# Performance work log

Hardware: AMD Instinct MI355X
Metric: run time of the kernel (lower is better)

Reference implementation:

```python
import jax, jax.numpy as jnp
import numpy as np

B, T, E, H = 4, 2048, 1024, 16
HS = E // H  # head_size = 64
FFN_HID = 100  # hard-coded in FeedForward
EPS = 1e-5


def layernorm(x, g, b):
    mu = jnp.mean(x, axis=-1, keepdims=True)
    var = jnp.mean(jnp.square(x - mu), axis=-1, keepdims=True)
    return (x - mu) * jax.lax.rsqrt(var + EPS) * g + b


def setup_inputs() -> dict:
    key = jax.random.key(0)
    ks = jax.random.split(key, 10)
    s = E ** -0.5
    return {
        "x": jax.random.normal(ks[0], (B, T, E), jnp.float32),
        "wq": jax.random.normal(ks[1], (E, E), jnp.float32) * s,
        "wk": jax.random.normal(ks[2], (E, E), jnp.float32) * s,
        "wv": jax.random.normal(ks[3], (E, E), jnp.float32) * s,
        "w_proj": jax.random.normal(ks[4], (E, E), jnp.float32) * s,
        "b_proj": jnp.zeros((E,), jnp.float32),
        "w1": jax.random.normal(ks[5], (E, FFN_HID), jnp.float32) * s,
        "b1": jnp.zeros((FFN_HID,), jnp.float32),
        "w2": jax.random.normal(ks[6], (FFN_HID, E), jnp.float32) * (FFN_HID ** -0.5),
        "b2": jnp.zeros((E,), jnp.float32),
        "ln1_g": jnp.ones((E,), jnp.float32),
        "ln1_b": jnp.zeros((E,), jnp.float32),
        "ln2_g": jnp.ones((E,), jnp.float32),
        "ln2_b": jnp.zeros((E,), jnp.float32),
    }


def reference(x, wq, wk, wv, w_proj, b_proj, w1, b1, w2, b2, ln1_g, ln1_b, ln2_g, ln2_b):
    # --- self-attention with pre-LN residual ---
    h = layernorm(x, ln1_g, ln1_b)  # [B,T,E]
    def split_heads(y):  # [B,T,E] -> [B,H,T,HS]
        return y.reshape(B, T, H, HS).transpose(0, 2, 1, 3)
    q = split_heads(h @ wq)
    k = split_heads(h @ wk)
    v = split_heads(h @ wv)
    # NOTE: original scales by C**-0.5 with C = n_embd (not head_size)
    wei = jnp.einsum("bhtd,bhsd->bhts", q, k) * (E ** -0.5)  # [B,H,T,T]
    causal = jnp.tril(jnp.ones((T, T), bool))
    wei = jnp.where(causal, wei, -jnp.inf)
    wei = jax.nn.softmax(wei, axis=-1)
    att = jnp.einsum("bhts,bhsd->bhtd", wei, v)  # [B,H,T,HS]
    att = att.transpose(0, 2, 1, 3).reshape(B, T, E)  # concat heads
    x = x + att @ w_proj + b_proj
    # --- feedforward with pre-LN residual ---
    h2 = layernorm(x, ln2_g, ln2_b)
    ff = jax.nn.relu(h2 @ w1 + b1) @ w2 + b2
    return x + ff
```

## Files before the change

kernel.cpp:

```cpp
#include <hip/hip_runtime.h>

typedef unsigned short u16;
typedef unsigned int u32;
typedef __bf16 bf16x8 __attribute__((ext_vector_type(8)));
typedef float f32x4 __attribute__((ext_vector_type(4)));

#define BDIM 4
#define TDIM 2048
#define EDIM 1024
#define HDIM 16
#define HS 64
#define MROWS (BDIM * TDIM)
#define FFNP 128

__device__ __forceinline__ u16 f2bf(float f) {
    __bf16 h = (__bf16)f;
    return __builtin_bit_cast(u16, h);
}

__device__ __forceinline__ void glds16(const void* g, void* l) {
    __builtin_amdgcn_global_load_lds(
        (__attribute__((address_space(1))) const void*)g,
        (__attribute__((address_space(3))) void*)l, 16, 0, 0);
}

__global__ __launch_bounds__(256) void transpose4(
    const float* __restrict__ s0, const float* __restrict__ s1,
    const float* __restrict__ s2, const float* __restrict__ s3,
    u16* __restrict__ d0, u16* __restrict__ d1,
    u16* __restrict__ d2, u16* __restrict__ d3)
{
    __shared__ u16 sm[64][72];
    const float* src; u16* dst;
    switch (blockIdx.z) {
        case 0: src = s0; dst = d0; break;
        case 1: src = s1; dst = d1; break;
        case 2: src = s2; dst = d2; break;
        default: src = s3; dst = d3; break;
    }
    int k0 = blockIdx.x * 64, n0 = blockIdx.y * 64;
    int tid = threadIdx.x;
#pragma unroll
    for (int i = 0; i < 16; i++) {
        int idx = i * 256 + tid;
        int kl = idx >> 6, nl = idx & 63;
        sm[kl][nl] = f2bf(src[(size_t)(k0 + kl) * EDIM + n0 + nl]);
    }
    __syncthreads();
#pragma unroll
    for (int i = 0; i < 16; i++) {
        int idx = i * 256 + tid;
        int nl = idx >> 6, kl = idx & 63;
        dst[(size_t)(n0 + nl) * EDIM + k0 + kl] = sm[kl][nl];
    }
}

__global__ __launch_bounds__(256) void transpose_pad(
    const float* __restrict__ src, u16* __restrict__ dst,
    int K, int N, int Kpad, int Npad)
{
    __shared__ u16 sm[64][72];
    int k0 = blockIdx.x * 64, n0 = blockIdx.y * 64;
    int tid = threadIdx.x;
#pragma unroll
    for (int i = 0; i < 16; i++) {
        int idx = i * 256 + tid;
        int kl = idx >> 6, nl = idx & 63;
        int k = k0 + kl, n = n0 + nl;
        float v = (k < K && n < N) ? src[(size_t)k * N + n] : 0.f;
        sm[kl][nl] = f2bf(v);
    }
    __syncthreads();
#pragma unroll
    for (int i = 0; i < 16; i++) {
        int idx = i * 256 + tid;
        int nl = idx >> 6, kl = idx & 63;
        int n = n0 + nl, k = k0 + kl;
        if (n < Npad && k < Kpad) dst[(size_t)n * Kpad + k] = sm[kl][nl];
    }
}

__global__ __launch_bounds__(256) void ln_rows(
    const float* __restrict__ X, const float* __restrict__ G,
    const float* __restrict__ Bv, u16* __restrict__ H)
{
    int w = threadIdx.x >> 6, l = threadIdx.x & 63;
    int row = blockIdx.x * 4 + w;
    const float* xr = X + (size_t)row * EDIM;
    float4 v[4];
    float s = 0.f, s2 = 0.f;
#pragma unroll
    for (int i = 0; i < 4; i++) {
        v[i] = *(const float4*)&xr[l * 4 + i * 256];
        s += v[i].x + v[i].y + v[i].z + v[i].w;
        s2 += v[i].x * v[i].x + v[i].y * v[i].y + v[i].z * v[i].z + v[i].w * v[i].w;
    }
#pragma unroll
    for (int off = 1; off < 64; off <<= 1) {
        s += __shfl_xor(s, off, 64);
        s2 += __shfl_xor(s2, off, 64);
    }
    float mean = s * (1.f / EDIM);
    float var = s2 * (1.f / EDIM) - mean * mean;
    float rstd = rsqrtf(var + 1e-5f);
#pragma unroll
    for (int i = 0; i < 4; i++) {
        int c = l * 4 + i * 256;
        float4 gg = *(const float4*)&G[c];
        float4 bb = *(const float4*)&Bv[c];
        u16 o0 = f2bf((v[i].x - mean) * rstd * gg.x + bb.x);
        u16 o1 = f2bf((v[i].y - mean) * rstd * gg.y + bb.y);
        u16 o2 = f2bf((v[i].z - mean) * rstd * gg.z + bb.z);
        u16 o3 = f2bf((v[i].w - mean) * rstd * gg.w + bb.w);
        uint2 pk;
        pk.x = (u32)o0 | ((u32)o1 << 16);
        pk.y = (u32)o2 | ((u32)o3 << 16);
        *(uint2*)&H[(size_t)row * EDIM + c] = pk;
    }
}

#define LDA4(d, mfb)                                                          \
    _Pragma("unroll") for (int mi = 0; mi < 4; mi++)                          \
    _Pragma("unroll") for (int ks = 0; ks < 2; ks++)                          \
        a[mi][ks] = *(const bf16x8*)&L[d][0][wm][((mfb + mi) * 16 + lr) * 64  \
                        + (((lg + 4 * ks) ^ (lr & 7)) << 3)];
#define LDB2(d, nfb)                                                          \
    _Pragma("unroll") for (int ni = 0; ni < 2; ni++)                          \
    _Pragma("unroll") for (int ks = 0; ks < 2; ks++)                          \
        b[ni][ks] = *(const bf16x8*)&L[d][1][wh][((wn & 1) * 64               \
                        + (nfb + ni) * 16 + lr) * 64                          \
                        + (((lg + 4 * ks) ^ (lr & 7)) << 3)];
#define MFMAQ(mfb, nfb)                                                       \
    _Pragma("unroll") for (int mi = 0; mi < 4; mi++)                          \
    _Pragma("unroll") for (int ni = 0; ni < 2; ni++)                          \
    _Pragma("unroll") for (int ks = 0; ks < 2; ks++)                          \
        acc[mfb + mi][nfb + ni] = __builtin_amdgcn_mfma_f32_16x16x32_bf16(    \
            a[mi][ks], b[ni][ks], acc[mfb + mi][nfb + ni], 0, 0, 0);
#define PH_SYNC1()                                                            \
    __builtin_amdgcn_s_barrier();                                             \
    asm volatile("s_waitcnt lgkmcnt(0)" ::: "memory");                        \
    __builtin_amdgcn_sched_barrier(0);                                        \
    __builtin_amdgcn_s_setprio(1);
#define PH_SYNC2()                                                            \
    __builtin_amdgcn_s_setprio(0);                                            \
    __builtin_amdgcn_s_barrier();
#define PH_SYNC2V(cond)                                                       \
    __builtin_amdgcn_s_setprio(0);                                            \
    if (cond) { asm volatile("s_waitcnt vmcnt(2)" ::: "memory"); }            \
    else      { asm volatile("s_waitcnt vmcnt(0)" ::: "memory"); }            \
    __builtin_amdgcn_s_barrier();

template <int MODE>
__global__ __launch_bounds__(512, 2) void gemm256(
    const u16* __restrict__ A, const u16* __restrict__ Bt,
    u16* __restrict__ Cb, float* __restrict__ Cf,
    const float* __restrict__ resid, const float* __restrict__ bias,
    int M, int N, int K, int lda, int ldb, int mb)
{
    __shared__ u16 L[2][2][2][128 * 64];
    const u16 *pA, *pB;
    int LA, LB, NN, bx, by;
    bool vmode = false;
    if constexpr (MODE == 5) {
        int id = blockIdx.x;
        if (id < 256) {
            int sw = (id & 7) * 32 + (id >> 3);
            bx = sw % 32; by = sw / 32;
            pA = A; pB = Bt; LA = 1024; LB = 1024; NN = 2048;
        } else {
            id -= 256;
            int sw = (id & 7) * 16 + (id >> 3);
            bx = sw % 4; by = sw / 4;
            pA = Bt + (size_t)2048 * 1024;
            pB = A;
            LA = 1024; LB = 1024; NN = 8192;
            vmode = true;
        }
    } else {
        int nwg = gridDim.x, id = blockIdx.x;
        int sw = (id & 7) * (nwg >> 3) + (id >> 3);
        bx = sw % mb; by = sw / mb;
        pA = A; pB = Bt; LA = lda; LB = ldb; NN = N;
    }
    const int m0 = bx * 256, n0 = by * 256;

    const int tid = threadIdx.x;
    const int w = tid >> 6, l = tid & 63;
    const int wm = w >> 2, wn = w & 3, wh = wn >> 1;
    const int lg = l >> 4, lr = l & 15;

    const int srow = w * 16 + (l >> 3);
    const int sch8 = ((l & 7) ^ (l >> 3)) * 8;

    auto stA = [&](int d, int h, int t) {
        const u16* src = pA + (size_t)(m0 + h * 128 + srow) * LA + t * 64 + sch8;
        u16* dst = &L[d][0][h][w * 1024];
        glds16(src, dst);
        glds16(src + (size_t)8 * LA, dst + 512);
    };
    auto stB = [&](int d, int h, int t) {
        const u16* src = pB + (size_t)(n0 + h * 128 + srow) * LB + t * 64 + sch8;
        u16* dst = &L[d][1][h][w * 1024];
        glds16(src, dst);
        glds16(src + (size_t)8 * LB, dst + 512);
    };

    f32x4 acc[8][4];
#pragma unroll
    for (int i = 0; i < 8; i++)
#pragma unroll
        for (int j = 0; j < 4; j++) acc[i][j] = f32x4{0.f, 0.f, 0.f, 0.f};
    bf16x8 a[4][2], b[2][2];

    const int NI = K >> 7;

    stA(0, 0, 0); stA(0, 1, 0); stB(0, 0, 0); stB(0, 1, 0);
    stB(1, 0, 1);
    asm volatile("s_waitcnt vmcnt(2)" ::: "memory");
    __builtin_amdgcn_s_barrier();

#pragma unroll 1
    for (int j = 0; j < NI; j++) {
        const int t = 2 * j;
        const bool more = (j + 1 < NI);
        LDA4(0, 0); LDB2(0, 0);
        stA(1, 0, t + 1);
        PH_SYNC1(); MFMAQ(0, 0); PH_SYNC2();
        LDA4(0, 4);
        stA(1, 1, t + 1);
        PH_SYNC1(); MFMAQ(4, 0); PH_SYNC2();
        LDB2(0, 2);
        stB(1, 1, t + 1);
        PH_SYNC1(); MFMAQ(4, 2); PH_SYNC2();
        LDA4(0, 0);
        if (more) stB(0, 1, t + 2);
        PH_SYNC1(); MFMAQ(0, 2); PH_SYNC2V(more);
        LDA4(1, 0); LDB2(1, 0);
        if (more) stA(0, 0, t + 2);
        PH_SYNC1(); MFMAQ(0, 0); PH_SYNC2();
        LDA4(1, 4);
        if (more) stA(0, 1, t + 2);
        PH_SYNC1(); MFMAQ(4, 0); PH_SYNC2();
        LDB2(1, 2);
        if (more) stB(0, 0, t + 2);
        PH_SYNC1(); MFMAQ(4, 2); PH_SYNC2();
        LDA4(1, 0);
        if (more) stB(1, 0, t + 3);
        PH_SYNC1(); MFMAQ(0, 2); PH_SYNC2V(more);
    }

#pragma unroll
    for (int mf = 0; mf < 8; mf++) {
#pragma unroll
        for (int nf = 0; nf < 4; nf++) {
#pragma unroll
            for (int e = 0; e < 4; e++) {
                int row = m0 + wm * 128 + mf * 16 + lg * 4 + e;
                int col = n0 + wn * 64 + nf * 16 + lr;
                float v = acc[mf][nf][e];
                if constexpr (MODE == 5) {
                    if (!vmode) {
                        Cb[(size_t)row * 2048 + col] = f2bf(v);
                    } else {
                        u16* vtp = (u16*)Cf;
                        int bq = col >> 11, tt = col & 2047;
                        vtp[((size_t)bq * 1024 + row) * 2048 + tt] = f2bf(v);
                    }
                } else {
                    size_t idx = (size_t)row * NN + col;
                    Cf[idx] = resid[idx] + v + bias[col];
                }
            }
        }
    }
}

template <int MODE>
__global__ __launch_bounds__(256, 2) void gemm_bt(
    const u16* __restrict__ A, const u16* __restrict__ Bt,
    u16* __restrict__ Cb, float* __restrict__ Cf,
    const float* __restrict__ resid, const float* __restrict__ bias,
    int M, int N, int K, int lda, int ldb, int mb)
{
    __shared__ u16 As[2][128 * 32];
    __shared__ u16 Bs[2][128 * 32];
    int bx, by;
    if constexpr (MODE == 4) {
        bx = blockIdx.x; by = blockIdx.y;
        int kz = blockIdx.z;
        A += kz * 256;
        Bt += kz * 256;
        Cf += (size_t)kz * M * N;
    } else {
        int nwg = gridDim.x, id = blockIdx.x;
        int sw = (id & 7) * (nwg >> 3) + (id >> 3);
        bx = sw % mb; by = sw / mb;
    }
    const int tid = threadIdx.x;
    const int w = tid >> 6, l = tid & 63;
    const int wr = w >> 1, wc = w & 1;
    const int lg = l >> 4, lr = l & 15;
    const int m0 = bx * 128, n0 = by * 128;

    f32x4 zero = {0.f, 0.f, 0.f, 0.f};
    f32x4 acc[4][4];
#pragma unroll
    for (int i = 0; i < 4; i++)
#pragma unroll
        for (int j = 0; j < 4; j++) acc[i][j] = zero;

    const u16* Ag = A + (size_t)(m0 + w * 16 + (l >> 2)) * lda + (l & 3) * 8;
    const u16* Bg = Bt + (size_t)(n0 + w * 16 + (l >> 2)) * ldb + (l & 3) * 8;

    auto stage = [&](int b, int k0) {
        glds16(Ag + k0, &As[b][w * 512]);
        glds16(Ag + k0 + (size_t)64 * lda, &As[b][w * 512 + 2048]);
        glds16(Bg + k0, &Bs[b][w * 512]);
        glds16(Bg + k0 + (size_t)64 * ldb, &Bs[b][w * 512 + 2048]);
    };
    auto compute = [&](int b) {
        bf16x8 af[4], bfr[4];
#pragma unroll
        for (int t = 0; t < 4; t++)
            af[t] = *(const bf16x8*)&As[b][(wr * 64 + t * 16 + lr) * 32 + lg * 8];
#pragma unroll
        for (int t = 0; t < 4; t++)
            bfr[t] = *(const bf16x8*)&Bs[b][(wc * 64 + t * 16 + lr) * 32 + lg * 8];
#pragma unroll
        for (int i = 0; i < 4; i++)
#pragma unroll
            for (int j = 0; j < 4; j++)
                acc[i][j] = __builtin_amdgcn_mfma_f32_16x16x32_bf16(
                    af[i], bfr[j], acc[i][j], 0, 0, 0);
    };

    stage(0, 0);
    __syncthreads();
    int cur = 0;
    for (int k0 = 32; k0 < K; k0 += 32) {
        stage(cur ^ 1, k0);
        compute(cur);
        __syncthreads();
        cur ^= 1;
    }
    compute(cur);

#pragma unroll
    for (int i = 0; i < 4; i++) {
#pragma unroll
        for (int j = 0; j < 4; j++) {
#pragma unroll
            for (int e = 0; e < 4; e++) {
                int row = m0 + wr * 64 + i * 16 + lg * 4 + e;
                int col = n0 + wc * 64 + j * 16 + lr;
                float v = acc[i][j][e];
                size_t idx = (size_t)row * N + col;
                if constexpr (MODE == 3) {
                    Cf[idx] = resid[idx] + v + bias[col];
                } else {
                    Cf[idx] = v;
                }
            }
        }
    }
}

__global__ __launch_bounds__(256) void relu_reduce4(
    const float* __restrict__ fp, const float* __restrict__ b1,
    u16* __restrict__ tb)
{
    const size_t CH = (size_t)MROWS * FFNP;
    size_t base = ((size_t)blockIdx.x * 256 + threadIdx.x) * 4;
    float4 s0 = *(const float4*)&fp[base];
    float4 s1 = *(const float4*)&fp[base + CH];
    float4 s2 = *(const float4*)&fp[base + 2 * CH];
    float4 s3 = *(const float4*)&fp[base + 3 * CH];
    int col = (int)(base & (FFNP - 1));
    float sv[4] = {s0.x + s1.x + s2.x + s3.x, s0.y + s1.y + s2.y + s3.y,
                   s0.z + s1.z + s2.z + s3.z, s0.w + s1.w + s2.w + s3.w};
    u16 o[4];
#pragma unroll
    for (int j = 0; j < 4; j++) {
        int c = col + j;
        float b = (c < 100) ? b1[c] : 0.f;
        o[j] = f2bf(fmaxf(sv[j] + b, 0.f));
    }
    uint2 pk;
    pk.x = (u32)o[0] | ((u32)o[1] << 16);
    pk.y = (u32)o[2] | ((u32)o[3] << 16);
    *(uint2*)&tb[base] = pk;
}

__global__ __launch_bounds__(256, 4) void attn_fwd(
    const u16* __restrict__ qk, const u16* __restrict__ Vt,
    u16* __restrict__ Og)
{
    int xcd = blockIdx.x & 7;
    int j = blockIdx.x >> 3;
    int bh = xcd * 8 + (j & 7);
    int qp = j >> 3;
    int bb = bh >> 4, hh = bh & 15;

    int tid = threadIdx.x;
    int w = tid >> 6, l = tid & 63;
    int lg = l >> 4, lr = l & 15;

    const u16* Qb = qk + ((size_t)bb * TDIM) * 2048 + hh * HS;
    const u16* Kb = Qb + 1024;
    const u16* Vb = Vt + (size_t)bh * HS * TDIM;

    __shared__ u16 Ks[2][64 * 64];
    __shared__ u16 Vs[2][64 * 64];
    __shared__ u16 Ps[4][16 * 64];

    int srow = w * 16 + (l >> 3);
    int schunk = (l & 7) ^ ((l >> 3) & 7);
    u16* Pw = Ps[w];
    int sbase = (l & 48) + lg * 4;

    const float QSCL = 0.045084227f;

#pragma unroll 1
    for (int qi = 0; qi < 2; qi++) {
        int qb = (qi == 0 ? qp : 31 - qp) * 64;
        int q_abs = qb + w * 16 + lr;
        int wlo = qb + w * 16;
        int nt = qb / 64 + 1;

        bf16x8 qf[2];
        qf[0] = *(const bf16x8*)&Qb[(size_t)q_abs * 2048 + lg * 8];
        qf[1] = *(const bf16x8*)&Qb[(size_t)q_abs * 2048 + 32 + lg * 8];
#pragma unroll
        for (int i = 0; i < 8; i++) {
            qf[0][i] = (__bf16)((float)qf[0][i] * QSCL);
            qf[1][i] = (__bf16)((float)qf[1][i] * QSCL);
        }

        f32x4 zero = {0.f, 0.f, 0.f, 0.f};
        f32x4 oacc[4];
#pragma unroll
        for (int dt = 0; dt < 4; dt++) oacc[dt] = zero;
        float lpart = 0.f;

        auto stage = [&](int b, int kv0) {
            glds16(Kb + (size_t)(kv0 + srow) * 2048 + schunk * 8, &Ks[b][w * 1024]);
            glds16(Kb + (size_t)(kv0 + srow + 8) * 2048 + schunk * 8,
                   &Ks[b][w * 1024 + 512]);
            glds16(Vb + (size_t)srow * TDIM + kv0 + schunk * 8, &Vs[b][w * 1024]);
            glds16(Vb + (size_t)(srow + 8) * TDIM + kv0 + schunk * 8,
                   &Vs[b][w * 1024 + 512]);
        };

        stage(0, 0);
        __syncthreads();
        int cur = 0;
#pragma unroll 1
        for (int t = 0; t < nt; t++) {
            int kv0 = t * 64;
            if (t + 1 < nt) stage(cur ^ 1, kv0 + 64);
            const u16* Kc = Ks[cur];
            const u16* Vc = Vs[cur];
            f32x4 sc[4];
#pragma unroll
            for (int ct = 0; ct < 4; ct++) sc[ct] = zero;
            __builtin_amdgcn_s_setprio(1);
#pragma unroll
            for (int ct = 0; ct < 4; ct++) {
#pragma unroll
                for (int dc = 0; dc < 2; dc++) {
                    bf16x8 kf = *(const bf16x8*)&Kc[(ct * 16 + lr) * 64 +
                                                    (((lg + 4 * dc) ^ (lr & 7)) << 3)];
                    sc[ct] = __builtin_amdgcn_mfma_f32_16x16x32_bf16(
                        kf, qf[dc], sc[ct], 0, 0, 0);
                }
            }
            __builtin_amdgcn_s_setprio(0);
            bf16x8 vfr[2][4];
#pragma unroll
            for (int m = 0; m < 2; m++)
#pragma unroll
                for (int dt = 0; dt < 4; dt++)
                    vfr[m][dt] = *(const bf16x8*)&Vc[(dt * 16 + lr) * 64 +
                                                     (((lg + 4 * m) ^ (lr & 7)) << 3)];
            float p[16];
            if (kv0 + 63 > wlo) {
#pragma unroll
                for (int ct = 0; ct < 4; ct++) {
#pragma unroll
                    for (int e = 0; e < 4; e++) {
                        float v = sc[ct][e];
                        if (kv0 + ct * 16 + lg * 4 + e > q_abs) v = -1e30f;
                        p[ct * 4 + e] = v;
                    }
                }
            } else {
#pragma unroll
                for (int ct = 0; ct < 4; ct++) {
#pragma unroll
                    for (int e = 0; e < 4; e++) p[ct * 4 + e] = sc[ct][e];
                }
            }
            float psum = 0.f;
#pragma unroll
            for (int i = 0; i < 16; i++) {
                p[i] = __builtin_amdgcn_exp2f(p[i]);
                psum += p[i];
            }
            lpart += psum;
#pragma unroll
            for (int ct = 0; ct < 4; ct++) {
#pragma unroll
                for (int i = 0; i < 2; i++) {
                    u32 word = (u32)f2bf(p[ct * 4 + 2 * i]) |
                               ((u32)f2bf(p[ct * 4 + 2 * i + 1]) << 16);
                    int kvb = ct * 16 + lg * 4 + 2 * i;
                    int idx = lr * 64 + ((((kvb >> 3) ^ (lr & 7)) << 3) | (kvb & 7));
                    *(u32*)&Pw[idx] = word;
                }
            }
            asm volatile("s_waitcnt lgkmcnt(0)" ::: "memory");
            __builtin_amdgcn_sched_barrier(0);
            __builtin_amdgcn_s_setprio(1);
#pragma unroll
            for (int m = 0; m < 2; m++) {
                bf16x8 pa = *(const bf16x8*)&Pw[lr * 64 + (((lg + 4 * m) ^ (lr & 7)) << 3)];
#pragma unroll
                for (int dt = 0; dt < 4; dt++) {
                    oacc[dt] = __builtin_amdgcn_mfma_f32_16x16x32_bf16(
                        pa, vfr[m][dt], oacc[dt], 0, 0, 0);
                }
            }
            __builtin_amdgcn_s_setprio(0);
            __syncthreads();
            cur ^= 1;
        }
        float lsum = lpart;
        lsum += __shfl_xor(lsum, 16, 64);
        lsum += __shfl_xor(lsum, 32, 64);
        float lT[4];
#pragma unroll
        for (int e = 0; e < 4; e++) lT[e] = __shfl(lsum, sbase + e, 64);
#pragma unroll
        for (int dt = 0; dt < 4; dt++) {
#pragma unroll
            for (int e = 0; e < 4; e++) {
                int row = qb + w * 16 + lg * 4 + e;
                Og[((size_t)bb * TDIM + row) * EDIM + hh * HS + dt * 16 + lr] =
                    f2bf(oacc[dt][e] / lT[e]);
            }
        }
    }
}

extern "C" void kernel_launch(void* const* d_in, const int* in_sizes, int n_in,
                              void* d_out, int out_size, void* d_ws, size_t ws_size,
                              hipStream_t stream)
{
    const float* x     = (const float*)d_in[0];
    const float* wq    = (const float*)d_in[1];
    const float* wk    = (const float*)d_in[2];
    const float* wv    = (const float*)d_in[3];
    const float* wproj = (const float*)d_in[4];
    const float* bproj = (const float*)d_in[5];
    const float* w1    = (const float*)d_in[6];
    const float* b1    = (const float*)d_in[7];
    const float* w2    = (const float*)d_in[8];
    const float* b2    = (const float*)d_in[9];
    const float* ln1g  = (const float*)d_in[10];
    const float* ln1b  = (const float*)d_in[11];
    const float* ln2g  = (const float*)d_in[12];
    const float* ln2b  = (const float*)d_in[13];
    float* out = (float*)d_out;

    char* ws = (char*)d_ws;
    size_t off = 0;
    auto alloc = [&](size_t bytes) -> void* {
        void* p = (void*)(ws + off);
        off += (bytes + 255) & ~(size_t)255;
        return p;
    };
    u16* hbuf = (u16*)alloc((size_t)MROWS * EDIM * 2);
    u16* qk   = (u16*)alloc((size_t)MROWS * 2048 * 2);
    u16* attb = (u16*)alloc((size_t)MROWS * EDIM * 2);
    u16* vt   = (u16*)alloc((size_t)MROWS * EDIM * 2);
    u16* wqkvt = (u16*)alloc((size_t)3072 * EDIM * 2);
    u16* wpt  = (u16*)alloc((size_t)EDIM * EDIM * 2);
    u16* w1t  = (u16*)alloc((size_t)FFNP * EDIM * 2);
    u16* w2t  = (u16*)alloc((size_t)EDIM * FFNP * 2);
    float* fp = (float*)qk;
    u16* tb   = vt;

    transpose4<<<dim3(16, 16, 4), 256, 0, stream>>>(
        wq, wk, wv, wproj,
        wqkvt, wqkvt + (size_t)EDIM * EDIM, wqkvt + (size_t)2 * EDIM * EDIM, wpt);
    transpose_pad<<<dim3(16, 2), 256, 0, stream>>>(w1, w1t, EDIM, 100, EDIM, FFNP);
    transpose_pad<<<dim3(2, 16), 256, 0, stream>>>(w2, w2t, 100, EDIM, FFNP, EDIM);

    ln_rows<<<MROWS / 4, 256, 0, stream>>>(x, ln1g, ln1b, hbuf);
    gemm256<5><<<dim3(384), 512, 0, stream>>>(hbuf, wqkvt, qk, (float*)vt,
                                              nullptr, nullptr,
                                              MROWS, 2048, EDIM, EDIM, EDIM, 32);
    attn_fwd<<<dim3(1024), 256, 0, stream>>>(qk, vt, attb);
    gemm256<1><<<dim3(128), 512, 0, stream>>>(attb, wpt, nullptr, out, x, bproj,
                                              MROWS, EDIM, EDIM, EDIM, EDIM, 32);
    ln_rows<<<MROWS / 4, 256, 0, stream>>>(out, ln2g, ln2b, hbuf);
    gemm_bt<4><<<dim3(64, 1, 4), 256, 0, stream>>>(hbuf, w1t, nullptr, fp, nullptr,
                                                   nullptr, MROWS, FFNP, 256, EDIM, EDIM, 64);
    relu_reduce4<<<dim3(MROWS * FFNP / 1024), 256, 0, stream>>>(fp, b1, tb);
    gemm_bt<3><<<dim3(512), 256, 0, stream>>>(tb, w2t, nullptr, out, out, b2,
                                              MROWS, EDIM, FFNP, FFNP, FFNP, 64);
}
```

Baseline: 236.5 us.

## Fuse split-K reduce and ReLU into FFN2 GEMM; deepen attention KV prefetch

Removes the separate relu_reduce4 kernel. The second FFN GEMM now reads the four split-K fp32 partials directly, sums them, adds b1, applies ReLU and converts to bf16 while staging its A tile. This drops one launch and the bf16 intermediate round-trip, but every N-tile block re-reads the fp32 partials (8 column blocks). The attention loop also moves to a two-ahead prefetch using explicit vmcnt waits and raw s_barrier in place of __syncthreads, so loads overlap more with compute.

```diff
diff --git a/kernel.cpp b/kernel.cpp
--- a/kernel.cpp
+++ b/kernel.cpp
@@ -353,42 +353,115 @@
             for (int e = 0; e < 4; e++) {
                 int row = m0 + wr * 64 + i * 16 + lg * 4 + e;
                 int col = n0 + wc * 64 + j * 16 + lr;
-                float v = acc[i][j][e];
                 size_t idx = (size_t)row * N + col;
-                if constexpr (MODE == 3) {
-                    Cf[idx] = resid[idx] + v + bias[col];
-                } else {
-                    Cf[idx] = v;
-                }
-            }
-        }
-    }
-}
-
-__global__ __launch_bounds__(256) void relu_reduce4(
-    const float* __restrict__ fp, const float* __restrict__ b1,
-    u16* __restrict__ tb)
-{
+                Cf[idx] = acc[i][j][e];
+            }
+        }
+    }
+}
+
+__global__ __launch_bounds__(256, 2) void ffn2_fused(
+    const float* __restrict__ fp, const u16* __restrict__ w2t,
+    const float* __restrict__ b1, const float* __restrict__ b2,
+    float* __restrict__ out)
+{
+    __shared__ u16 As[2][128 * 32];
+    __shared__ u16 Bs[2][128 * 32];
     const size_t CH = (size_t)MROWS * FFNP;
-    size_t base = ((size_t)blockIdx.x * 256 + threadIdx.x) * 4;
-    float4 s0 = *(const float4*)&fp[base];
-    float4 s1 = *(const float4*)&fp[base + CH];
-    float4 s2 = *(const float4*)&fp[base + 2 * CH];
-    float4 s3 = *(const float4*)&fp[base + 3 * CH];
-    int col = (int)(base & (FFNP - 1));
-    float sv[4] = {s0.x + s1.x + s2.x + s3.x, s0.y + s1.y + s2.y + s3.y,
-                   s0.z + s1.z + s2.z + s3.z, s0.w + s1.w + s2.w + s3.w};
-    u16 o[4];
-#pragma unroll
-    for (int j = 0; j < 4; j++) {
-        int c = col + j;
-        float b = (c < 100) ? b1[c] : 0.f;
-        o[j] = f2bf(fmaxf(sv[j] + b, 0.f));
-    }
-    uint2 pk;
-    pk.x = (u32)o[0] | ((u32)o[1] << 16);
-    pk.y = (u32)o[2] | ((u32)o[3] << 16);
-    *(uint2*)&tb[base] = pk;
+    int nwg = gridDim.x, id = blockIdx.x;
+    int sw = (id & 7) * (nwg >> 3) + (id >> 3);
+    int bx = sw % 64, by = sw / 64;
+    const int tid = threadIdx.x;
+    const int w = tid >> 6, l = tid & 63;
+    const int wr = w >> 1, wc = w & 1;
+    const int lg = l >> 4, lr = l & 15;
+    const int m0 = bx * 128, n0 = by * 128;
+
+    f32x4 zero = {0.f, 0.f, 0.f, 0.f};
+    f32x4 acc[4][4];
+#pragma unroll
+    for (int i = 0; i < 4; i++)
+#pragma unroll
+        for (int j = 0; j < 4; j++) acc[i][j] = zero;
+
+    const int arow = m0 + w * 16 + (l >> 2);
+    const int c0 = (l & 3) * 8;
+    const u16* Bg = w2t + (size_t)(n0 + w * 16 + (l >> 2)) * FFNP + c0;
+
+    auto stageA = [&](int b, int k0) {
+#pragma unroll
+        for (int rr = 0; rr < 2; rr++) {
+            int row = arow + rr * 64;
+            const float4* p = (const float4*)&fp[(size_t)row * FFNP + k0 + c0];
+            const size_t c4 = CH / 4;
+            float4 x0 = p[0],          x1 = p[1];
+            float4 y0 = p[c4],         y1 = p[c4 + 1];
+            float4 z0 = p[2 * c4],     z1 = p[2 * c4 + 1];
+            float4 q0 = p[3 * c4],     q1 = p[3 * c4 + 1];
+            float v[8] = {
+                x0.x + y0.x + z0.x + q0.x, x0.y + y0.y + z0.y + q0.y,
+                x0.z + y0.z + z0.z + q0.z, x0.w + y0.w + z0.w + q0.w,
+                x1.x + y1.x + z1.x + q1.x, x1.y + y1.y + z1.y + q1.y,
+                x1.z + y1.z + z1.z + q1.z, x1.w + y1.w + z1.w + q1.w };
+            u16 o[8];
+#pragma unroll
+            for (int jj = 0; jj < 8; jj++) {
+                int c = k0 + c0 + jj;
+                float bb = (c < 100) ? b1[c] : 0.f;
+                o[jj] = f2bf(fmaxf(v[jj] + bb, 0.f));
+            }
+            uint4 pk;
+            pk.x = (u32)o[0] | ((u32)o[1] << 16);
+            pk.y = (u32)o[2] | ((u32)o[3] << 16);
+            pk.z = (u32)o[4] | ((u32)o[5] << 16);
+            pk.w = (u32)o[6] | ((u32)o[7] << 16);
+            *(uint4*)&As[b][w * 512 + (l >> 2) * 32 + c0 + rr * 2048] = pk;
+        }
+    };
+    auto stageB = [&](int b, int k0) {
+        glds16(Bg + k0, &Bs[b][w * 512]);
+        glds16(Bg + k0 + (size_t)64 * FFNP, &Bs[b][w * 512 + 2048]);
+    };
+    auto compute = [&](int b) {
+        bf16x8 af[4], bfr[4];
+#pragma unroll
+        for (int t = 0; t < 4; t++)
+            af[t] = *(const bf16x8*)&As[b][(wr * 64 + t * 16 + lr) * 32 + lg * 8];
+#pragma unroll
+        for (int t = 0; t < 4; t++)
+            bfr[t] = *(const bf16x8*)&Bs[b][(wc * 64 + t * 16 + lr) * 32 + lg * 8];
+#pragma unroll
+        for (int i = 0; i < 4; i++)
+#pragma unroll
+            for (int j = 0; j < 4; j++)
+                acc[i][j] = __builtin_amdgcn_mfma_f32_16x16x32_bf16(
+                    af[i], bfr[j], acc[i][j], 0, 0, 0);
+    };
+
+    stageA(0, 0); stageB(0, 0);
+    __syncthreads();
+    int cur = 0;
+    for (int k0 = 32; k0 < FFNP; k0 += 32) {
+        stageA(cur ^ 1, k0); stageB(cur ^ 1, k0);
+        compute(cur);
+        __syncthreads();
+        cur ^= 1;
+    }
+    compute(cur);
+
+#pragma unroll
+    for (int i = 0; i < 4; i++) {
+#pragma unroll
+        for (int j = 0; j < 4; j++) {
+#pragma unroll
+            for (int e = 0; e < 4; e++) {
+                int row = m0 + wr * 64 + i * 16 + lg * 4 + e;
+                int col = n0 + wc * 64 + j * 16 + lr;
+                size_t idx = (size_t)row * EDIM + col;
+                out[idx] = out[idx] + acc[i][j][e] + b2[col];
+            }
+        }
+    }
 }
 
 __global__ __launch_bounds__(256, 4) void attn_fwd(
@@ -452,14 +525,17 @@
         };
 
         stage(0, 0);
-        __syncthreads();
-        int cur = 0;
+        if (nt > 1) stage(1, 64);
 #pragma unroll 1
         for (int t = 0; t < nt; t++) {
             int kv0 = t * 64;
-            if (t + 1 < nt) stage(cur ^ 1, kv0 + 64);
-            const u16* Kc = Ks[cur];
-            const u16* Vc = Vs[cur];
+            int buf = t & 1;
+            if (t + 1 < nt) { asm volatile("s_waitcnt vmcnt(4)" ::: "memory"); }
+            else            { asm volatile("s_waitcnt vmcnt(0)" ::: "memory"); }
+            __builtin_amdgcn_sched_barrier(0);
+            __builtin_amdgcn_s_barrier();
+            const u16* Kc = Ks[buf];
+            const u16* Vc = Vs[buf];
             f32x4 sc[4];
 #pragma unroll
             for (int ct = 0; ct < 4; ct++) sc[ct] = zero;
@@ -531,8 +607,8 @@
                 }
             }
             __builtin_amdgcn_s_setprio(0);
-            __syncthreads();
-            cur ^= 1;
+            __builtin_amdgcn_s_barrier();
+            if (t + 2 < nt) stage(buf, kv0 + 128);
         }
         float lsum = lpart;
         lsum += __shfl_xor(lsum, 16, 64);
@@ -588,7 +664,6 @@
     u16* w1t  = (u16*)alloc((size_t)FFNP * EDIM * 2);
     u16* w2t  = (u16*)alloc((size_t)EDIM * FFNP * 2);
     float* fp = (float*)qk;
-    u16* tb   = vt;
 
     transpose4<<<dim3(16, 16, 4), 256, 0, stream>>>(
         wq, wk, wv, wproj,
@@ -606,7 +681,5 @@
     ln_rows<<<MROWS / 4, 256, 0, stream>>>(out, ln2g, ln2b, hbuf);
     gemm_bt<4><<<dim3(64, 1, 4), 256, 0, stream>>>(hbuf, w1t, nullptr, fp, nullptr,
                                                    nullptr, MROWS, FFNP, 256, EDIM, EDIM, 64);
-    relu_reduce4<<<dim3(MROWS * FFNP / 1024), 256, 0, stream>>>(fp, b1, tb);
-    gemm_bt<3><<<dim3(512), 256, 0, stream>>>(tb, w2t, nullptr, out, out, b2,
-                                              MROWS, EDIM, FFNP, FFNP, FFNP, 64);
-}
+    ffn2_fused<<<dim3(512), 256, 0, stream>>>(fp, w2t, b1, b2, out);
+}
```

Result: slower. 246.6 us (+4.3%).
